# Kernel tuning notes

Measured on AMD Instinct MI355X. Metric: run time of the kernel, lower is better.

## Reference

```python
import jax, jax.numpy as jnp
import numpy as np

EPS = 1e-15  # matches torch_geometric.nn.dense.dmon_pool.EPS


def setup_inputs() -> dict:
    key = jax.random.key(0)
    k1, k2, k3, k4 = jax.random.split(key, 4)
    B, N, C, K = 8, 4096, 128, 64
    x = jax.random.normal(k1, (B, N, C), dtype=jnp.float32)
    adj = jax.random.uniform(k2, (B, N, N), dtype=jnp.float32)
    # Linear(C -> K) params of the cluster-assignment MLP
    weight = jax.random.normal(k3, (C, K), dtype=jnp.float32) / np.sqrt(C)
    bias = jax.random.normal(k4, (K,), dtype=jnp.float32) * 0.01
    return {"x": x, "adj": adj, "weight": weight, "bias": bias}


def reference(x, adj, weight, bias):
    B, N, C = x.shape
    K = weight.shape[1]
    dt = x.dtype

    # cluster assignment: linear + softmax (dropout = 0)
    s = jax.nn.softmax(x @ weight + bias, axis=-1)            # [B, N, K]

    # pooled features: selu(S^T X)
    out = jax.nn.selu(jnp.einsum('bnk,bnc->bkc', s, x))       # [B, K, C]

    # pooled adjacency: S^T A S
    sT_adj = jnp.einsum('bnk,bnm->bkm', s, adj)               # [B, K, N]
    out_adj = jnp.einsum('bkm,bml->bkl', sT_adj, s)           # [B, K, K]

    # spectral (modularity) loss
    deg = adj.sum(-1)                                         # [B, N]
    m = deg.sum(-1) / 2                                       # [B]
    ca = jnp.einsum('bnk,bn->bk', s, deg)                     # [B, K] (== cb)
    normalizer = ca[:, :, None] * ca[:, None, :] / 2 / m[:, None, None]
    decompose = out_adj - normalizer
    spectral_loss = (-jnp.trace(decompose, axis1=-2, axis2=-1) / 2 / m).mean()

    # orthogonality loss
    ss = jnp.einsum('bnk,bnl->bkl', s, s)                     # [B, K, K]
    ss_fro = jnp.linalg.norm(ss, axis=(-2, -1), keepdims=True)
    i_s = jnp.eye(K, dtype=dt)
    sqrt_k = jnp.sqrt(jnp.asarray(K, dt))
    ortho_loss = jnp.linalg.norm(ss / ss_fro - i_s / sqrt_k, axis=(-2, -1)).mean()

    # cluster-size loss (mask = all-ones, so mask.sum == N)
    cluster_size = s.sum(axis=1)                              # [B, K]
    cluster_loss = (jnp.linalg.norm(cluster_size, axis=1) / N * sqrt_k - 1).mean()

    # zero the diagonal, then symmetric degree-normalize the pooled adjacency
    out_adj = out_adj * (1.0 - i_s)
    d = jnp.sqrt(out_adj.sum(-1)) + EPS                       # [B, K]
    out_adj = out_adj / d[:, None, :] / d[:, :, None]

    return s, out, out_adj, spectral_loss, ortho_loss, cluster_loss
```

## Files before the change

### kernel.cpp

```cpp
#include <hip/hip_runtime.h>
#include <hip/hip_bf16.h>


typedef _Float16 f16x8 __attribute__((ext_vector_type(8)));
typedef float f32x4 __attribute__((ext_vector_type(4)));

#define MFMA16(a, b, c) __builtin_amdgcn_mfma_f32_16x16x32_f16((a), (b), (c), 0, 0, 0)

__device__ __forceinline__ void gld_lds16(const void* g, void* l) {
  __builtin_amdgcn_global_load_lds(
      (const __attribute__((address_space(1))) void*)g,
      (__attribute__((address_space(3))) void*)l, 16, 0, 0);
}

template <int NCHUNK>
__device__ __forceinline__ void stage_lds(const void* g, void* lbase, int tid) {
  char* ld = (char*)lbase + (tid >> 6) * 1024;
  const char* gs = (const char*)g + tid * 16;
#pragma unroll
  for (int p = 0; p < NCHUNK; ++p)
    gld_lds16(gs + p * 4096, ld + p * 4096);
}

__global__ __launch_bounds__(256) void k_assign(
    const float* __restrict__ x, const float* __restrict__ w,
    const float* __restrict__ bias, float* __restrict__ s_out,
    _Float16* __restrict__ sB) {
  __shared__ __align__(16) _Float16 wT[2][64][136];
  __shared__ __align__(16) float sT[64][76];
  const int b = blockIdx.x & 7;
  const int it = blockIdx.x >> 3;
  const int n_base = it * 64;
  const int tid = threadIdx.x;

  for (int idx = tid; idx < 8192; idx += 256) {
    int c = idx >> 6, k = idx & 63;
    float v = w[idx];
    _Float16 h = (_Float16)v;
    wT[0][k][c] = h;
    wT[1][k][c] = (_Float16)(v - (float)h);
  }
  const int l = tid & 63, wv = tid >> 6;
  const int l15 = l & 15, g = l >> 4;
  float bv[4];
#pragma unroll
  for (int ct = 0; ct < 4; ++ct) bv[ct] = bias[ct * 16 + l15];
  __syncthreads();

  f32x4 acc[4];
#pragma unroll
  for (int ct = 0; ct < 4; ++ct) acc[ct] = (f32x4){bv[ct], bv[ct], bv[ct], bv[ct]};

  const float* xrow = x + ((size_t)(b * 4096 + n_base + wv * 16 + l15)) * 128;
#pragma unroll
  for (int cs = 0; cs < 4; ++cs) {
    const int c0 = cs * 32;
    f32x4 r0 = *(const f32x4*)(xrow + c0 + 8 * g);
    f32x4 r1 = *(const f32x4*)(xrow + c0 + 8 * g + 4);
    f16x8 ah, al;
#pragma unroll
    for (int j = 0; j < 4; ++j) {
      float v0 = r0[j]; _Float16 h0 = (_Float16)v0;
      ah[j] = h0; al[j] = (_Float16)(v0 - (float)h0);
      float v1 = r1[j]; _Float16 h1 = (_Float16)v1;
      ah[4 + j] = h1; al[4 + j] = (_Float16)(v1 - (float)h1);
    }
#pragma unroll
    for (int ct = 0; ct < 4; ++ct) {
      f16x8 bh = *(const f16x8*)&wT[0][ct * 16 + l15][c0 + 8 * g];
      f16x8 bl = *(const f16x8*)&wT[1][ct * 16 + l15][c0 + 8 * g];
      acc[ct] = MFMA16(ah, bh, acc[ct]);
      acc[ct] = MFMA16(al, bh, acc[ct]);
      acc[ct] = MFMA16(ah, bl, acc[ct]);
    }
  }

#pragma unroll
  for (int r = 0; r < 4; ++r) {
    float m = fmaxf(fmaxf(acc[0][r], acc[1][r]), fmaxf(acc[2][r], acc[3][r]));
#pragma unroll
    for (int off = 1; off < 16; off <<= 1) m = fmaxf(m, __shfl_xor(m, off, 64));
    float e[4], sum = 0.f;
#pragma unroll
    for (int ct = 0; ct < 4; ++ct) { e[ct] = __expf(acc[ct][r] - m); sum += e[ct]; }
#pragma unroll
    for (int off = 1; off < 16; off <<= 1) sum += __shfl_xor(sum, off, 64);
    float inv = 1.0f / sum;
#pragma unroll
    for (int ct = 0; ct < 4; ++ct) acc[ct][r] = e[ct] * inv;
  }

  const int row_l = wv * 16 + 4 * g;
  float* srow = s_out + ((size_t)(b * 4096 + n_base)) * 64;
#pragma unroll
  for (int r = 0; r < 4; ++r)
#pragma unroll
    for (int ct = 0; ct < 4; ++ct) {
      srow[(size_t)(row_l + r) * 64 + ct * 16 + l15] = acc[ct][r];
      sT[ct * 16 + l15][row_l + r] = acc[ct][r];
    }
  __syncthreads();

  _Float16* dst = sB + (size_t)(b * 64 + it) * 4096;
#pragma unroll
  for (int p = 0; p < 2; ++p) {
    int slot = tid + 256 * p;
    int ks = slot >> 8, ct = (slot >> 6) & 3, ln = slot & 63;
    int col = ct * 16 + (ln & 15);
    int row0 = ks * 32 + 8 * (ln >> 4);
    f16x8 o;
#pragma unroll
    for (int j = 0; j < 8; ++j) o[j] = (_Float16)sT[col][row0 + j];
    *(f16x8*)(dst + slot * 8) = o;
  }
}

__global__ __launch_bounds__(512, 4) void k_big(
    const float* __restrict__ adj, const _Float16* __restrict__ sB,
    const float* __restrict__ s_out, float* __restrict__ oadj_part) {
  __shared__ __align__(16) float sl[4096];
  __shared__ __align__(16) float Yl[4096];
  const int b = blockIdx.x & 7;
  const int nt = blockIdx.x >> 3;
  const int n_base = nt * 64;
  const int tid = threadIdx.x;
  const int l = tid & 63, w = tid >> 6;
  const int wr = w & 3, kh = w >> 2;
  const int l15 = l & 15, g = l >> 4;

  {
    char* ld = (char*)sl + w * 1024;
    const char* gs =
        (const char*)(s_out + ((size_t)(b * 4096 + n_base)) * 64) + tid * 16;
    gld_lds16(gs, ld);
    gld_lds16(gs + 8192, ld + 8192);
  }

  const f16x8* fbase =
      (const f16x8*)(sB + (size_t)b * 64 * 4096) + (size_t)kh * 32 * 512 + l;
  const float* arow = adj + ((size_t)b * 4096 + n_base + wr * 16 + l15) * 4096 +
                      kh * 2048 + 8 * g;

  f32x4 A0, A1, A2, A3, B0, B1, B2, B3;
  A0 = *(const f32x4*)(arow);        A1 = *(const f32x4*)(arow + 4);
  A2 = *(const f32x4*)(arow + 32);   A3 = *(const f32x4*)(arow + 36);
  B0 = *(const f32x4*)(arow + 64);   B1 = *(const f32x4*)(arow + 68);
  B2 = *(const f32x4*)(arow + 96);   B3 = *(const f32x4*)(arow + 100);

  f32x4 acc[4] = {};

  auto phase = [&](f32x4& C0, f32x4& C1, f32x4& C2, f32x4& C3, int p) {
    const f16x8* fb = fbase + (size_t)p * 512;
    f16x8 F[8];
#pragma unroll
    for (int q = 0; q < 8; ++q) F[q] = fb[q * 64];
    f16x8 a0, a1;
#pragma unroll
    for (int j = 0; j < 4; ++j) {
      a0[j] = (_Float16)C0[j]; a0[4 + j] = (_Float16)C1[j];
      a1[j] = (_Float16)C2[j]; a1[4 + j] = (_Float16)C3[j];
    }
    if (p + 2 < 32) {
      const float* an = arow + (p + 2) * 64;
      C0 = *(const f32x4*)(an);       C1 = *(const f32x4*)(an + 4);
      C2 = *(const f32x4*)(an + 32);  C3 = *(const f32x4*)(an + 36);
    }
#pragma unroll
    for (int ct = 0; ct < 4; ++ct) acc[ct] = MFMA16(a0, F[ct], acc[ct]);
#pragma unroll
    for (int ct = 0; ct < 4; ++ct) acc[ct] = MFMA16(a1, F[4 + ct], acc[ct]);
  };

#pragma unroll 2
  for (int p = 0; p < 32; p += 2) {
    phase(A0, A1, A2, A3, p);
    phase(B0, B1, B2, B3, p + 1);
  }

  if (kh == 0) {
#pragma unroll
    for (int r = 0; r < 4; ++r)
#pragma unroll
      for (int ct = 0; ct < 4; ++ct)
        Yl[(wr * 16 + 4 * g + r) * 64 + ct * 16 + l15] = acc[ct][r];
  }
  __syncthreads();
  if (kh == 1) {
#pragma unroll
    for (int r = 0; r < 4; ++r)
#pragma unroll
      for (int ct = 0; ct < 4; ++ct)
        Yl[(wr * 16 + 4 * g + r) * 64 + ct * 16 + l15] += acc[ct][r];
  }
  __syncthreads();

  const int kq = tid >> 4, lq = tid & 15;
  f32x4 a2a = {}, a2b = {};
  for (int r = 0; r < 64; ++r) {
    float sA = sl[r * 64 + kq];
    float sC = sl[r * 64 + 32 + kq];
    f32x4 y4 = *(const f32x4*)(Yl + r * 64 + lq * 4);
#pragma unroll
    for (int j = 0; j < 4; ++j) { a2a[j] += sA * y4[j]; a2b[j] += sC * y4[j]; }
  }
  float* op = oadj_part + ((size_t)(b * 64 + nt)) * 4096;
  *(f32x4*)(op + kq * 64 + lq * 4) = a2a;
  *(f32x4*)(op + (kq + 32) * 64 + lq * 4) = a2b;
}

__global__ __launch_bounds__(256) void k_small(
    const float* __restrict__ s_out, const float* __restrict__ x,
    float* __restrict__ ss_part, float* __restrict__ p_part,
    float* __restrict__ csp) {
  __shared__ __align__(16) float sc[32 * 64];
  __shared__ __align__(16) float xc[32 * 128];
  __shared__ float qc[4][64];
  const int b = blockIdx.x & 7;
  const int ch = blockIdx.x >> 3;
  const int tid = threadIdx.x;
  const int kq = tid >> 4, cq = tid & 15;
  const int kk = tid & 63, nq = tid >> 6;
  f32x4 ssa[4] = {};
  f32x4 pa[8] = {};
  float csA = 0.f;
  for (int sub = 0; sub < 8; ++sub) {
    if (sub) __syncthreads();
    const int nb = ch * 256 + sub * 32;
    stage_lds<2>(s_out + ((size_t)(b * 4096 + nb)) * 64, sc, tid);
    stage_lds<4>(x + ((size_t)(b * 4096 + nb)) * 128, xc, tid);
    __syncthreads();
    for (int n = 0; n < 32; ++n) {
      f32x4 s4 = *(const f32x4*)(sc + n * 64 + kq * 4);
      f32x4 s4b = *(const f32x4*)(sc + n * 64 + cq * 4);
      f32x4 x4a = *(const f32x4*)(xc + n * 128 + cq * 8);
      f32x4 x4b = *(const f32x4*)(xc + n * 128 + cq * 8 + 4);
#pragma unroll
      for (int i = 0; i < 4; ++i) {
#pragma unroll
        for (int j = 0; j < 4; ++j) {
          ssa[i][j] += s4[i] * s4b[j];
          pa[i * 2][j] += s4[i] * x4a[j];
          pa[i * 2 + 1][j] += s4[i] * x4b[j];
        }
      }
    }
    for (int n = nq; n < 32; n += 4) csA += sc[n * 64 + kk];
  }
  float* sp = ss_part + ((size_t)(b * 16 + ch)) * 4096;
  float* pp = p_part + ((size_t)(b * 16 + ch)) * 8192;
#pragma unroll
  for (int i = 0; i < 4; ++i) {
    *(f32x4*)(sp + (kq * 4 + i) * 64 + cq * 4) = ssa[i];
    *(f32x4*)(pp + (kq * 4 + i) * 128 + cq * 8) = pa[i * 2];
    *(f32x4*)(pp + (kq * 4 + i) * 128 + cq * 8 + 4) = pa[i * 2 + 1];
  }
  __syncthreads();
  qc[nq][kk] = csA;
  __syncthreads();
  if (tid < 64)
    csp[(size_t)(b * 16 + ch) * 64 + tid] =
        qc[0][tid] + qc[1][tid] + qc[2][tid] + qc[3][tid];
}

__global__ __launch_bounds__(256) void k_reduce(
    const float* __restrict__ oadj_part, const float* __restrict__ ss_part,
    const float* __restrict__ p_part, float* __restrict__ oadj_raw,
    float* __restrict__ ss_sum, float* __restrict__ out_feat) {
  const int gid = blockIdx.x * 256 + threadIdx.x;
  if (gid < 32768) {
    int b = gid >> 12, e = gid & 4095;
    float s = 0.f;
    for (int t = 0; t < 64; ++t) s += oadj_part[((size_t)(b * 64 + t)) * 4096 + e];
    oadj_raw[gid] = s;
  } else if (gid < 65536) {
    int g2 = gid - 32768, b = g2 >> 12, e = g2 & 4095;
    float s = 0.f;
    for (int t = 0; t < 16; ++t) s += ss_part[((size_t)(b * 16 + t)) * 4096 + e];
    ss_sum[g2] = s;
  } else {
    int g3 = gid - 65536, b = g3 >> 13, e = g3 & 8191;
    float s = 0.f;
    for (int t = 0; t < 16; ++t) s += p_part[((size_t)(b * 16 + t)) * 8192 + e];
    const float scale = 1.0507009873554805f, alpha = 1.6732632423543772f;
    out_feat[g3] = s > 0.f ? scale * s : scale * alpha * (expf(s) - 1.f);
  }
}

__global__ __launch_bounds__(256) void k_finalize(
    const float* __restrict__ oadj_raw, const float* __restrict__ ss_sum,
    const float* __restrict__ csp, float* __restrict__ out_adj,
    float* __restrict__ loss_part) {
  __shared__ float red[256];
  __shared__ float ca[64], dvec[64], diag[64];
  const int b = blockIdx.x, t = threadIdx.x;
  const float* ob = oadj_raw + b * 4096;
  const float* ssb = ss_sum + b * 4096;

  if (t < 64) {
    const float* orow = ob + t * 64;
    float full = 0.f, nod = 0.f;
    for (int lc = 0; lc < 64; ++lc) {
      float v = orow[lc];
      full += v;
      nod += (lc != t) ? v : 0.f;
    }
    ca[t] = full;
    dvec[t] = sqrtf(nod) + 1e-15f;
    diag[t] = orow[t];
  }
  __syncthreads();

  red[t] = (t < 64) ? ca[t] : 0.f;
  __syncthreads();
  for (int o = 128; o > 0; o >>= 1) { if (t < o) red[t] += red[t + o]; __syncthreads(); }
  const float sm = red[0];
  __syncthreads();

  red[t] = (t < 64) ? (diag[t] - ca[t] * ca[t] / sm) : 0.f;
  __syncthreads();
  for (int o = 128; o > 0; o >>= 1) { if (t < o) red[t] += red[t + o]; __syncthreads(); }
  const float spectral_b = -red[0] / sm;
  __syncthreads();

  float fp = 0.f;
  for (int i = t; i < 4096; i += 256) { float v = ssb[i]; fp += v * v; }
  red[t] = fp; __syncthreads();
  for (int o = 128; o > 0; o >>= 1) { if (t < o) red[t] += red[t + o]; __syncthreads(); }
  const float fro = sqrtf(red[0]);
  __syncthreads();
  float op2 = 0.f;
  for (int i = t; i < 4096; i += 256) {
    float v = ssb[i] / fro - (((i >> 6) == (i & 63)) ? 0.125f : 0.f);
    op2 += v * v;
  }
  red[t] = op2; __syncthreads();
  for (int o = 128; o > 0; o >>= 1) { if (t < o) red[t] += red[t + o]; __syncthreads(); }
  const float ortho_b = sqrtf(red[0]);
  __syncthreads();

  float csize_k = 0.f;
  if (t < 64) {
    for (int ch = 0; ch < 16; ++ch) csize_k += csp[(size_t)(b * 16 + ch) * 64 + t];
  }
  red[t] = (t < 64) ? csize_k * csize_k : 0.f;
  __syncthreads();
  for (int o = 128; o > 0; o >>= 1) { if (t < o) red[t] += red[t + o]; __syncthreads(); }
  const float cluster_b = sqrtf(red[0]) * 8.f / 4096.f - 1.f;
  __syncthreads();

  for (int i = t; i < 4096; i += 256) {
    int kk = i >> 6, lc = i & 63;
    float v = (kk == lc) ? 0.f : ob[i] / (dvec[kk] * dvec[lc]);
    out_adj[(size_t)b * 4096 + i] = v;
  }
  if (t == 0) {
    loss_part[b * 3 + 0] = spectral_b;
    loss_part[b * 3 + 1] = ortho_b;
    loss_part[b * 3 + 2] = cluster_b;
  }
}

__global__ void k_scalars(const float* __restrict__ lp, float* __restrict__ o3) {
  if (threadIdx.x == 0) {
    float s = 0.f, o = 0.f, c = 0.f;
    for (int b = 0; b < 8; ++b) { s += lp[b * 3]; o += lp[b * 3 + 1]; c += lp[b * 3 + 2]; }
    o3[0] = s * 0.125f; o3[1] = o * 0.125f; o3[2] = c * 0.125f;
  }
}

extern "C" void kernel_launch(void* const* d_in, const int* in_sizes, int n_in,
                              void* d_out, int out_size, void* d_ws, size_t ws_size,
                              hipStream_t stream) {
  const float* x = (const float*)d_in[0];
  const float* adj = (const float*)d_in[1];
  const float* w = (const float*)d_in[2];
  const float* bias = (const float*)d_in[3];
  float* out = (float*)d_out;
  float* s_out = out;
  float* out_feat = out + 2097152;
  float* out_adj = out + 2162688;
  float* out_sc = out + 2195456;

  char* ws = (char*)d_ws;
  _Float16* sB = (_Float16*)ws;
  float* oadj_part = (float*)(ws + (8u << 20));
  float* ss_part = (float*)(ws + (16u << 20));
  float* p_part = (float*)(ws + (20u << 20));
  float* oadj_raw = (float*)(ws + (28u << 20) + (128u << 10));
  float* ss_sum = (float*)(ws + (28u << 20) + (256u << 10));
  float* loss_part = (float*)(ws + (28u << 20) + (384u << 10));
  float* csp = (float*)(ws + (28u << 20) + (512u << 10));

  k_assign<<<dim3(512), dim3(256), 0, stream>>>(x, w, bias, s_out, sB);
  k_big<<<dim3(512), dim3(512), 0, stream>>>(adj, sB, s_out, oadj_part);
  k_small<<<dim3(128), dim3(256), 0, stream>>>(s_out, x, ss_part, p_part, csp);
  k_reduce<<<dim3(512), dim3(256), 0, stream>>>(oadj_part, ss_part, p_part,
                                                oadj_raw, ss_sum, out_feat);
  k_finalize<<<dim3(8), dim3(256), 0, stream>>>(oadj_raw, ss_sum, csp,
                                                out_adj, loss_part);
  k_scalars<<<dim3(1), dim3(64), 0, stream>>>(loss_part, out_sc);
}
```

Baseline: 209.8 us.

## Stage adj and S tiles through triple-buffered LDS with async global-to-LDS loads

The main adj·S loop in k_big now streams adj rows and S fragments into a three-deep LDS ring using global_load_lds with an XOR swizzle, instead of loading adj directly into registers with a two-deep register prefetch. Waves now split the K columns (two column tiles each) rather than the reduction dimension, so the LDS cross-wave add of partial Y is removed. The aim is deeper memory latency hiding and fewer registers on this bandwidth-bound read of adj. In exchange the block uses 72 KB of LDS, which can cut the number of resident blocks, and adds a barrier on every step.

```diff
diff --git a/kernel.cpp b/kernel.cpp
--- a/kernel.cpp
+++ b/kernel.cpp
@@ -118,79 +118,89 @@
 __global__ __launch_bounds__(512, 4) void k_big(
     const float* __restrict__ adj, const _Float16* __restrict__ sB,
     const float* __restrict__ s_out, float* __restrict__ oadj_part) {
-  __shared__ __align__(16) float sl[4096];
-  __shared__ __align__(16) float Yl[4096];
+  __shared__ __align__(16) char pool[73728];
   const int b = blockIdx.x & 7;
   const int nt = blockIdx.x >> 3;
   const int n_base = nt * 64;
   const int tid = threadIdx.x;
   const int l = tid & 63, w = tid >> 6;
-  const int wr = w & 3, kh = w >> 2;
-  const int l15 = l & 15, g = l >> 4;
+  const int rt = w & 3, ch = w >> 2;
+  const int g = l >> 4;
+
+  const char* sBb = (const char*)(sB + (size_t)b * 64 * 4096);
+  const char* asrc = (const char*)adj +
+      ((size_t)(b * 4096 + n_base + (tid >> 4)) * 4096) * 4 +
+      (((tid & 15) * 16) ^ (((tid >> 4) & 7) << 4));
+  const size_t CH1 = (size_t)32 * 16384;
+  const char* fsrc = sBb + tid * 16;
+
+  auto stage = [&](int s, int buf) {
+    char* ab = pool + buf * 16384 + w * 1024;
+    const char* a0 = asrc + (size_t)s * 256;
+    gld_lds16(a0, ab);
+    gld_lds16(a0 + CH1, ab + 8192);
+    gld_lds16(fsrc + (size_t)s * 8192, pool + 49152 + buf * 8192 + w * 1024);
+  };
+
+  stage(0, 0);
+  stage(1, 1);
+
+  const int rowbase = (rt * 16 + (l & 15)) * 256;
+  const int swz = (l & 7) << 4;
+  int innerX[4];
+#pragma unroll
+  for (int ks = 0; ks < 2; ++ks)
+#pragma unroll
+    for (int part = 0; part < 2; ++part)
+      innerX[ks * 2 + part] = (ks * 128 + g * 32 + part * 16) ^ swz;
+
+  f32x4 acc[2] = {};
+  int buf = 0;
+  for (int s = 0; s < 64; ++s) {
+    if (s == 63) asm volatile("s_waitcnt vmcnt(0)" ::: "memory");
+    else         asm volatile("s_waitcnt vmcnt(3)" ::: "memory");
+    __builtin_amdgcn_sched_barrier(0);
+    __builtin_amdgcn_s_barrier();
+    if (s < 62) {
+      int nb = buf + 2; if (nb >= 3) nb -= 3;
+      stage(s + 2, nb);
+    }
+    const char* ab = pool + buf * 16384;
+    const char* fbb = pool + 49152 + buf * 8192;
+#pragma unroll
+    for (int ks = 0; ks < 2; ++ks) {
+      f32x4 lo = *(const f32x4*)(ab + rowbase + innerX[ks * 2]);
+      f32x4 hi = *(const f32x4*)(ab + rowbase + innerX[ks * 2 + 1]);
+      f16x8 af;
+#pragma unroll
+      for (int j = 0; j < 4; ++j) {
+        af[j] = (_Float16)lo[j];
+        af[4 + j] = (_Float16)hi[j];
+      }
+      f16x8 b0 = *(const f16x8*)(fbb + (ks * 4 + ch * 2 + 0) * 1024 + l * 16);
+      f16x8 b1 = *(const f16x8*)(fbb + (ks * 4 + ch * 2 + 1) * 1024 + l * 16);
+      acc[0] = MFMA16(af, b0, acc[0]);
+      acc[1] = MFMA16(af, b1, acc[1]);
+    }
+    buf = (buf == 2) ? 0 : buf + 1;
+  }
 
   {
-    char* ld = (char*)sl + w * 1024;
-    const char* gs =
-        (const char*)(s_out + ((size_t)(b * 4096 + n_base)) * 64) + tid * 16;
-    gld_lds16(gs, ld);
-    gld_lds16(gs + 8192, ld + 8192);
-  }
-
-  const f16x8* fbase =
-      (const f16x8*)(sB + (size_t)b * 64 * 4096) + (size_t)kh * 32 * 512 + l;
-  const float* arow = adj + ((size_t)b * 4096 + n_base + wr * 16 + l15) * 4096 +
-                      kh * 2048 + 8 * g;
-
-  f32x4 A0, A1, A2, A3, B0, B1, B2, B3;
-  A0 = *(const f32x4*)(arow);        A1 = *(const f32x4*)(arow + 4);
-  A2 = *(const f32x4*)(arow + 32);   A3 = *(const f32x4*)(arow + 36);
-  B0 = *(const f32x4*)(arow + 64);   B1 = *(const f32x4*)(arow + 68);
-  B2 = *(const f32x4*)(arow + 96);   B3 = *(const f32x4*)(arow + 100);
-
-  f32x4 acc[4] = {};
-
-  auto phase = [&](f32x4& C0, f32x4& C1, f32x4& C2, f32x4& C3, int p) {
-    const f16x8* fb = fbase + (size_t)p * 512;
-    f16x8 F[8];
-#pragma unroll
-    for (int q = 0; q < 8; ++q) F[q] = fb[q * 64];
-    f16x8 a0, a1;
-#pragma unroll
-    for (int j = 0; j < 4; ++j) {
-      a0[j] = (_Float16)C0[j]; a0[4 + j] = (_Float16)C1[j];
-      a1[j] = (_Float16)C2[j]; a1[4 + j] = (_Float16)C3[j];
-    }
-    if (p + 2 < 32) {
-      const float* an = arow + (p + 2) * 64;
-      C0 = *(const f32x4*)(an);       C1 = *(const f32x4*)(an + 4);
-      C2 = *(const f32x4*)(an + 32);  C3 = *(const f32x4*)(an + 36);
-    }
-#pragma unroll
-    for (int ct = 0; ct < 4; ++ct) acc[ct] = MFMA16(a0, F[ct], acc[ct]);
-#pragma unroll
-    for (int ct = 0; ct < 4; ++ct) acc[ct] = MFMA16(a1, F[4 + ct], acc[ct]);
-  };
-
-#pragma unroll 2
-  for (int p = 0; p < 32; p += 2) {
-    phase(A0, A1, A2, A3, p);
-    phase(B0, B1, B2, B3, p + 1);
-  }
-
-  if (kh == 0) {
+    const char* ssrc =
+        (const char*)(s_out + (size_t)(b * 4096 + n_base) * 64) + tid * 16;
+    gld_lds16(ssrc, pool + 16384 + w * 1024);
+    gld_lds16(ssrc + 8192, pool + 16384 + w * 1024 + 8192);
+  }
+  __syncthreads();
+
+  float* Yl = (float*)pool;
+  float* sl = (float*)(pool + 16384);
+#pragma unroll
+  for (int c2 = 0; c2 < 2; ++c2) {
+    const int ct = ch * 2 + c2;
 #pragma unroll
     for (int r = 0; r < 4; ++r)
-#pragma unroll
-      for (int ct = 0; ct < 4; ++ct)
-        Yl[(wr * 16 + 4 * g + r) * 64 + ct * 16 + l15] = acc[ct][r];
-  }
-  __syncthreads();
-  if (kh == 1) {
-#pragma unroll
-    for (int r = 0; r < 4; ++r)
-#pragma unroll
-      for (int ct = 0; ct < 4; ++ct)
-        Yl[(wr * 16 + 4 * g + r) * 64 + ct * 16 + l15] += acc[ct][r];
+      Yl[(rt * 16 + (l >> 4) * 4 + r) * 64 + ct * 16 + (l & 15)] = acc[c2][r];
   }
   __syncthreads();
 
```

New measurement: 186.0 us. -11.4%, faster.
